# Kernel optimization log

Measured on AMD Instinct MI355X. Metric: run time of the kernel, lower is better.

## Reference

```python
import jax, jax.numpy as jnp
import numpy as np
from jax import lax

DN = ('NCHW', 'OIHW', 'NCHW')
BN_EPS = 1e-5

def conv2d(x, w, b=None, pad=0):
    y = lax.conv_general_dilated(x, w, (1, 1), [(pad, pad), (pad, pad)], dimension_numbers=DN)
    if b is not None:
        y = y + b[None, :, None, None]
    return y

def setup_inputs() -> dict:
    key = jax.random.key(0)
    ks = jax.random.split(key, 12)
    B, C, H, W = 8, 256, 64, 64
    ca = C // 4  # dim_att = 64
    s = 0.05  # weight scale to keep attention logits sane
    return {
        'x': jax.random.normal(ks[0], (B, C, H, W), jnp.float32),
        'w_dw1': jax.random.normal(ks[1], (ca // 2, ca, 7, 7), jnp.float32) * s,
        'b_dw1': jax.random.normal(ks[2], (ca // 2,), jnp.float32) * s,
        'w_dw2': jax.random.normal(ks[3], (ca // 2, ca, 11, 11), jnp.float32) * s,
        'b_dw2': jax.random.normal(ks[4], (ca // 2,), jnp.float32) * s,
        'w_k': jax.random.normal(ks[5], (ca, ca, 1, 1), jnp.float32) * s,
        'b_k': jax.random.normal(ks[6], (ca,), jnp.float32) * s,
        'w_v': jax.random.normal(ks[7], (ca, ca, 1, 1), jnp.float32) * s,
        'b_v': jax.random.normal(ks[8], (ca,), jnp.float32) * s,
        'w_c1': jax.random.normal(ks[9], (C, C, 1, 1), jnp.float32) * s,
        'bn_g': jnp.ones((C,), jnp.float32),
        'bn_b': jnp.zeros((C,), jnp.float32),
        'bn_m': jnp.zeros((C,), jnp.float32),
        'bn_var': jnp.ones((C,), jnp.float32),
        'w_c2': jax.random.normal(ks[10], (C, C, 1, 1), jnp.float32) * s,
        'b_c2': jax.random.normal(ks[11], (C,), jnp.float32) * s,
    }

def reference(x, w_dw1, b_dw1, w_dw2, b_dw2, w_k, b_k, w_v, b_v,
              w_c1, bn_g, bn_b, bn_m, bn_var, w_c2, b_c2):
    ca = w_k.shape[0]  # dim_att
    B, C, H, W = x.shape
    HW = H * W
    x1 = x[:, :ca]
    x2 = x[:, ca:]
    # Q from two multi-scale convs (7x7 and 11x11, same padding)
    q = jnp.concatenate([conv2d(x1, w_dw1, b_dw1, pad=3),
                         conv2d(x1, w_dw2, b_dw2, pad=5)], axis=1)  # [B,ca,H,W]
    q = q.reshape(B, ca, HW)                                         # [B,ca,HW]
    k = conv2d(x1, w_k, b_k).reshape(B, ca, HW)                      # [B,ca,HW]
    v = conv2d(x1, w_v, b_v).reshape(B, ca, HW)                      # [B,ca,HW]
    # att[b,n,m] = softmax_m( sum_c q[b,c,n] * k[b,c,m] )
    att = jax.nn.softmax(jnp.einsum('bcn,bcm->bnm', q, k), axis=-1)  # [B,HW,HW]
    # out1[b,c,n] = sum_m v[b,c,m] * att[b,n,m]
    out1 = jnp.einsum('bcm,bnm->bcn', v, att).reshape(B, ca, H, W)
    y = jnp.concatenate([out1, x2], axis=1)  # [B,C,H,W]
    # conv1 = YOLO Conv: 1x1 conv (no bias) + BatchNorm (eval stats) + SiLU
    y = conv2d(y, w_c1)
    inv = lax.rsqrt(bn_var + BN_EPS)
    y = (y - bn_m[None, :, None, None]) * (bn_g * inv)[None, :, None, None] + bn_b[None, :, None, None]
    y = jax.nn.silu(y)
    # conv2 = plain 1x1 conv with bias
    return conv2d(y, w_c2, b_c2)
```

## Files before the change

### kernel.cpp

```cpp
#include <hip/hip_runtime.h>

typedef __attribute__((ext_vector_type(8))) short frag8;
typedef __attribute__((ext_vector_type(4))) float f32x4;
typedef __attribute__((ext_vector_type(8))) unsigned short us8;
typedef __attribute__((ext_vector_type(4))) unsigned short us4;
typedef __attribute__((ext_vector_type(2))) unsigned int u32x2;

#define MFMA(a,b,c) __builtin_amdgcn_mfma_f32_16x16x32_bf16((a),(b),(c),0,0,0)
#define LOG2E 1.44269504f
#define EXP2(x) __builtin_amdgcn_exp2f(x)

__device__ __forceinline__ unsigned short f2bf(float f){
  unsigned int u = __builtin_bit_cast(unsigned int, f);
  u += 0x7fffu + ((u >> 16) & 1u);
  return (unsigned short)(u >> 16);
}

__device__ __forceinline__ float bf2f(unsigned short h){
  unsigned int u = ((unsigned int)h) << 16;
  return __builtin_bit_cast(float, u);
}

__device__ __forceinline__ unsigned int cvt_pk_bf16(float a, float b){
  unsigned int r;
  asm volatile("v_cvt_pk_bf16_f32 %0, %1, %2" : "=v"(r) : "v"(a), "v"(b));
  return r;
}

#define OFF_XT   ((size_t)0)
#define OFF_KT   ((size_t)16777216)
#define OFF_VCT  ((size_t)20971520)
#define OFF_QT   ((size_t)25165824)
#define OFF_O1T  ((size_t)29360128)
#define OFF_ZT   ((size_t)33554432)
#define OFF_WQ7  ((size_t)50331648)
#define OFF_WQ11 ((size_t)50532352)
#define OFF_WC1  ((size_t)51027968)
#define OFF_WC2  ((size_t)51159040)
#define OFF_BC1  ((size_t)51290112)
#define OFF_WKB  ((size_t)51291136)
#define OFF_WVB  ((size_t)51299328)
#define OFF_ML2  OFF_WQ7
#define OFF_ML4  ((size_t)51307520)
#define WS_NEED4 ((size_t)(OFF_ML4 + 1048576))

__global__ __launch_bounds__(256) void prep_weights_kernel(
    const float* __restrict__ wdw1, const float* __restrict__ wdw2,
    const float* __restrict__ wc1, const float* __restrict__ bng,
    const float* __restrict__ bnb, const float* __restrict__ bnm,
    const float* __restrict__ bnv, const float* __restrict__ wc2,
    const float* __restrict__ wk, const float* __restrict__ wv,
    unsigned short* __restrict__ wq7, unsigned short* __restrict__ wq11,
    unsigned short* __restrict__ wc1b, unsigned short* __restrict__ wc2b,
    float* __restrict__ bc1, unsigned short* __restrict__ wkb,
    unsigned short* __restrict__ wvb){
  int i = blockIdx.x*256 + threadIdx.x;
  if (i < 100352){
    int o = i >> 11, rem = i & 2047;
    int co = rem >> 6, ci = rem & 63;
    int kh = o / 7, kw = o % 7;
    wq7[i] = f2bf(wdw1[(co*64 + ci)*49 + kh*7 + kw]);
  } else if (i < 348160){
    int j = i - 100352;
    int o = j >> 11, rem = j & 2047;
    int co = rem >> 6, ci = rem & 63;
    int kh = o / 11, kw = o % 11;
    wq11[j] = f2bf(wdw2[(co*64 + ci)*121 + kh*11 + kw]);
  } else if (i < 413696){
    int j = i - 348160;
    int co = j >> 8;
    float a = bng[co] * rsqrtf(bnv[co] + 1e-5f);
    wc1b[j] = f2bf(wc1[j] * a);
    if ((j & 255) == 0) bc1[co] = bnb[co] - bnm[co]*a;
  } else if (i < 479232){
    int j = i - 413696;
    wc2b[j] = f2bf(wc2[j]);
  } else if (i < 483328){
    int j = i - 479232;
    wkb[j] = f2bf(wk[j]);
  } else if (i < 487424){
    int j = i - 483328;
    wvb[j] = f2bf(wv[j]);
  }
}

__global__ __launch_bounds__(256) void prep_x_kernel(const float* __restrict__ x,
                                                     unsigned short* __restrict__ xt){
  int g = blockIdx.x*256 + threadIdx.x;
  int b = g >> 12, n = g & 4095;
  int c0base = blockIdx.y * 64;
  const float* xp = x + (((size_t)b*256) << 12) + n;
  unsigned short* op = xt + (size_t)g*256;
  for (int c0 = c0base; c0 < c0base + 64; c0 += 8){
    us8 v;
    #pragma unroll
    for (int j = 0; j < 8; ++j) v[j] = f2bf(xp[(size_t)(c0+j) << 12]);
    *reinterpret_cast<us8*>(op + c0) = v;
  }
}

__global__ __launch_bounds__(256) void kv_kernel(const unsigned short* __restrict__ xt,
    const unsigned short* __restrict__ wkb, const unsigned short* __restrict__ wvb,
    const float* __restrict__ bk, const float* __restrict__ bv,
    unsigned short* __restrict__ kt, unsigned short* __restrict__ vct){
  int gid = blockIdx.x;
  int part = gid >> 9, t = gid & 511;
  int b = t >> 6, tile = t & 63;
  int lane = threadIdx.x & 63, wid = threadIdx.x >> 6;
  int lo = lane & 15, hi = lane >> 4;
  int n0 = tile*64 + wid*16;
  size_t bb = (size_t)b << 12;
  f32x4 acc[4];
  #pragma unroll
  for (int f = 0; f < 4; ++f) acc[f] = (f32x4){0.f,0.f,0.f,0.f};
  frag8 x0 = *reinterpret_cast<const frag8*>(xt + (bb + n0 + lo)*256 + 8*hi);
  frag8 x1 = *reinterpret_cast<const frag8*>(xt + (bb + n0 + lo)*256 + 32 + 8*hi);
  if (part == 0){
    #pragma unroll
    for (int nf = 0; nf < 4; ++nf){
      frag8 w0 = *reinterpret_cast<const frag8*>(wkb + (nf*16 + lo)*64 + 8*hi);
      frag8 w1 = *reinterpret_cast<const frag8*>(wkb + (nf*16 + lo)*64 + 32 + 8*hi);
      acc[nf] = MFMA(x0, w0, acc[nf]);
      acc[nf] = MFMA(x1, w1, acc[nf]);
    }
    #pragma unroll
    for (int nf = 0; nf < 4; ++nf){
      int co = nf*16 + lo;
      float bias = bk[co];
      #pragma unroll
      for (int r = 0; r < 4; ++r)
        kt[(bb + n0 + hi*4 + r)*64 + co] = f2bf(acc[nf][r] + bias);
    }
  } else {
    #pragma unroll
    for (int mf = 0; mf < 4; ++mf){
      frag8 w0 = *reinterpret_cast<const frag8*>(wvb + (mf*16 + lo)*64 + 8*hi);
      frag8 w1 = *reinterpret_cast<const frag8*>(wvb + (mf*16 + lo)*64 + 32 + 8*hi);
      acc[mf] = MFMA(w0, x0, acc[mf]);
      acc[mf] = MFMA(w1, x1, acc[mf]);
    }
    #pragma unroll
    for (int mf = 0; mf < 4; ++mf){
      #pragma unroll
      for (int r = 0; r < 4; ++r){
        int c = mf*16 + hi*4 + r;
        vct[(((size_t)b*64 + c) << 12) + n0 + lo] = f2bf(acc[mf][r] + bv[c]);
      }
    }
  }
}

template<int KS>
__global__ __launch_bounds__(256) void conv_q_kernel(const unsigned short* __restrict__ xt,
    const unsigned short* __restrict__ wq, const float* __restrict__ bias,
    unsigned short* __restrict__ qt){
  constexpr int P = KS/2;
  constexpr int NR = (KS+1)/2;
  __shared__ unsigned short xs[NR*64*64];
  __shared__ float outst[2][64][33];
  int h0 = blockIdx.x*2, b = blockIdx.y;
  int tid = threadIdx.x, lane = tid & 63, wid = tid >> 6;
  int lo = lane & 15, hi = lane >> 4;
  int cofrag = wid & 1, hsel = wid >> 1;
  int h = h0 + hsel;
  f32x4 acc[4];
  #pragma unroll
  for (int nf = 0; nf < 4; ++nf) acc[nf] = (f32x4){0.f,0.f,0.f,0.f};
  const size_t xbase = ((size_t)b << 12) * 256;
  #pragma unroll
  for (int pass = 0; pass < 2; ++pass){
    const int srcBase = h0 - P + pass*NR;
    if (pass) __syncthreads();
    for (int idx = tid; idx < NR*512; idx += 256){
      int rl = idx >> 9, w = (idx >> 3) & 63, ch = idx & 7;
      int sr = srcBase + rl;
      us8 v = {0,0,0,0,0,0,0,0};
      if (sr >= 0 && sr < 64)
        v = *reinterpret_cast<const us8*>(xt + xbase + (size_t)(sr*64 + w)*256 + ch*8);
      int byte = (rl*64 + w)*128 + ((ch*16) ^ ((w & 7) << 4));
      *reinterpret_cast<us8*>((char*)xs + byte) = v;
    }
    __syncthreads();
    for (int rl = 0; rl < NR; ++rl){
      int dh = srcBase + rl - h + P;
      if (dh < 0 || dh >= KS) continue;
      frag8 wf[KS][2];
      int off0 = dh*KS;
      #pragma unroll
      for (int dw = 0; dw < KS; ++dw){
        #pragma unroll
        for (int ks = 0; ks < 2; ++ks)
          wf[dw][ks] = *reinterpret_cast<const frag8*>(
              wq + (size_t)(off0+dw)*2048 + (cofrag*16 + lo)*64 + ks*32 + 8*hi);
      }
      #pragma unroll
      for (int dw = 0; dw < KS; ++dw){
        #pragma unroll
        for (int nf = 0; nf < 4; ++nf){
          int w_out = nf*16 + lo;
          int wp = w_out + dw - P;
          frag8 bx0 = {0,0,0,0,0,0,0,0}, bx1 = {0,0,0,0,0,0,0,0};
          if (wp >= 0 && wp < 64){
            int rowb = (rl*64 + wp)*128;
            int sw = (wp & 7) << 4;
            bx0 = *reinterpret_cast<const frag8*>((char*)xs + rowb + ((hi*16) ^ sw));
            bx1 = *reinterpret_cast<const frag8*>((char*)xs + rowb + ((64 + hi*16) ^ sw));
          }
          acc[nf] = MFMA(wf[dw][0], bx0, acc[nf]);
          acc[nf] = MFMA(wf[dw][1], bx1, acc[nf]);
        }
      }
    }
  }
  #pragma unroll
  for (int nf = 0; nf < 4; ++nf){
    int w = nf*16 + lo;
    #pragma unroll
    for (int r = 0; r < 4; ++r)
      outst[hsel][w][cofrag*16 + hi*4 + r] = acc[nf][r];
  }
  __syncthreads();
  {
    int hs = tid >> 7, rem = tid & 127;
    int w = rem >> 1, c16 = (rem & 1)*16;
    int cobase = (KS == 7) ? 0 : 32;
    size_t qrow = (((size_t)b << 12) + (h0 + hs)*64 + w)*64;
    #pragma unroll
    for (int g = 0; g < 2; ++g){
      int c8 = c16 + g*8;
      us8 v;
      #pragma unroll
      for (int j = 0; j < 8; ++j)
        v[j] = f2bf((outst[hs][w][c8 + j] + bias[c8 + j]) * LOG2E);
      *reinterpret_cast<us8*>(qt + qrow + cobase + c8) = v;
    }
  }
}

template<int NSPLIT>
__global__ __launch_bounds__(256, 2) void attn_kernel(const unsigned short* __restrict__ qt,
    const unsigned short* __restrict__ kt, const unsigned short* __restrict__ vct,
    unsigned short* __restrict__ opart, float* __restrict__ mlpart){
  constexpr int TILES = 64 / NSPLIT;
  __shared__ unsigned short kls[2][64*64];
  __shared__ unsigned short vls[2][64*64];
  __shared__ unsigned short pls[4][32*64];
  int b = blockIdx.y, half = blockIdx.z;
  int tid = threadIdx.x, lane = tid & 63, wid = tid >> 6;
  int lo = lane & 15, hi = lane >> 4;
  int q0 = blockIdx.x*128 + wid*32;
  const size_t bb = (size_t)b << 12;
  const int mtbase = half * TILES;
  const int sm = tid >> 3, sch = tid & 7;
  const int dstA = sm*128 + ((sch*16) ^ ((sm & 7) << 4));
  const int dstB = dstA + 32*128;
  char* pbase = (char*)pls[wid];
  frag8 aq[2][2];
  #pragma unroll
  for (int mf = 0; mf < 2; ++mf)
    #pragma unroll
    for (int ks = 0; ks < 2; ++ks)
      aq[mf][ks] = *reinterpret_cast<const frag8*>(
          qt + (bb + q0 + mf*16 + lo)*64 + ks*32 + 8*hi);
  f32x4 o[2][4];
  #pragma unroll
  for (int mf = 0; mf < 2; ++mf)
    #pragma unroll
    for (int f = 0; f < 4; ++f) o[mf][f] = (f32x4){0.f,0.f,0.f,0.f};
  float mr[2]  = {-1e30f, -1e30f};
  float lr[2]  = {0.f, 0.f};
  float mrT[2][4];
  #pragma unroll
  for (int mf = 0; mf < 2; ++mf)
    #pragma unroll
    for (int r = 0; r < 4; ++r) mrT[mf][r] = -1e30f;
  us8 kr0, kr1, vr0, vr1;
  {
    int mt = mtbase;
    kr0 = *reinterpret_cast<const us8*>(kt + (bb + mt*64 + sm)*64 + sch*8);
    kr1 = *reinterpret_cast<const us8*>(kt + (bb + mt*64 + sm + 32)*64 + sch*8);
    vr0 = *reinterpret_cast<const us8*>(vct + (((size_t)b*64 + sm) << 12) + mt*64 + sch*8);
    vr1 = *reinterpret_cast<const us8*>(vct + (((size_t)b*64 + sm + 32) << 12) + mt*64 + sch*8);
    *reinterpret_cast<us8*>((char*)kls[0] + dstA) = kr0;
    *reinterpret_cast<us8*>((char*)kls[0] + dstB) = kr1;
    *reinterpret_cast<us8*>((char*)vls[0] + dstA) = vr0;
    *reinterpret_cast<us8*>((char*)vls[0] + dstB) = vr1;
  }
  __syncthreads();
  int cur = 0;
  for (int t = 0; t < TILES; ++t){
    if (t < TILES-1){
      int mt = mtbase + t + 1;
      kr0 = *reinterpret_cast<const us8*>(kt + (bb + mt*64 + sm)*64 + sch*8);
      kr1 = *reinterpret_cast<const us8*>(kt + (bb + mt*64 + sm + 32)*64 + sch*8);
      vr0 = *reinterpret_cast<const us8*>(vct + (((size_t)b*64 + sm) << 12) + mt*64 + sch*8);
      vr1 = *reinterpret_cast<const us8*>(vct + (((size_t)b*64 + sm + 32) << 12) + mt*64 + sch*8);
    }
    f32x4 s[2][4];
    #pragma unroll
    for (int mf = 0; mf < 2; ++mf)
      #pragma unroll
      for (int f = 0; f < 4; ++f) s[mf][f] = (f32x4){0.f,0.f,0.f,0.f};
    #pragma unroll
    for (int nf = 0; nf < 4; ++nf){
      int m = nf*16 + lo;
      int sw = (m & 7) << 4;
      frag8 b0 = *reinterpret_cast<const frag8*>((char*)kls[cur] + m*128 + ((hi*16) ^ sw));
      frag8 b1 = *reinterpret_cast<const frag8*>((char*)kls[cur] + m*128 + ((64 + hi*16) ^ sw));
      s[0][nf] = MFMA(b0, aq[0][0], s[0][nf]);
      s[0][nf] = MFMA(b1, aq[0][1], s[0][nf]);
      s[1][nf] = MFMA(b0, aq[1][0], s[1][nf]);
      s[1][nf] = MFMA(b1, aq[1][1], s[1][nf]);
    }
    float pm[2];
    #pragma unroll
    for (int mf = 0; mf < 2; ++mf){
      float a0 = fmaxf(fmaxf(s[mf][0][0], s[mf][0][1]), fmaxf(s[mf][0][2], s[mf][0][3]));
      float a1 = fmaxf(fmaxf(s[mf][1][0], s[mf][1][1]), fmaxf(s[mf][1][2], s[mf][1][3]));
      float a2 = fmaxf(fmaxf(s[mf][2][0], s[mf][2][1]), fmaxf(s[mf][2][2], s[mf][2][3]));
      float a3 = fmaxf(fmaxf(s[mf][3][0], s[mf][3][1]), fmaxf(s[mf][3][2], s[mf][3][3]));
      pm[mf] = fmaxf(fmaxf(a0, a1), fmaxf(a2, a3));
    }
    float growth = fmaxf(pm[0] - mr[0], pm[1] - mr[1]);
    if (!__all(growth <= 11.5416f)){
      float rmax[2] = {pm[0], pm[1]};
      #pragma unroll
      for (int mf = 0; mf < 2; ++mf){
        rmax[mf] = fmaxf(rmax[mf], __shfl_xor(rmax[mf], 16));
        rmax[mf] = fmaxf(rmax[mf], __shfl_xor(rmax[mf], 32));
        float mn = fmaxf(mr[mf], rmax[mf]);
        lr[mf] *= EXP2(mr[mf] - mn);
        mr[mf] = mn;
      }
      #pragma unroll
      for (int mf = 0; mf < 2; ++mf)
        #pragma unroll
        for (int r = 0; r < 4; ++r){
          float mnT = __shfl(mr[mf], hi*4 + r);
          float scT = EXP2(mrT[mf][r] - mnT);
          mrT[mf][r] = mnT;
          #pragma unroll
          for (int cf = 0; cf < 4; ++cf) o[mf][cf][r] *= scT;
        }
    }
    #pragma unroll
    for (int mf = 0; mf < 2; ++mf){
      float acc = 0.f;
      #pragma unroll
      for (int nf = 0; nf < 4; ++nf){
        #pragma unroll
        for (int r = 0; r < 4; ++r){
          s[mf][nf][r] = EXP2(s[mf][nf][r] - mr[mf]);
          acc += s[mf][nf][r];
        }
        u32x2 w;
        w[0] = cvt_pk_bf16(s[mf][nf][0], s[mf][nf][1]);
        w[1] = cvt_pk_bf16(s[mf][nf][2], s[mf][nf][3]);
        *reinterpret_cast<u32x2*>(pbase + (mf*16 + lo)*128 +
            ((nf*32 + hi*8) ^ ((lo & 7) << 4))) = w;
      }
      lr[mf] += acc;
    }
    #pragma unroll
    for (int ks = 0; ks < 2; ++ks){
      frag8 ap0 = *reinterpret_cast<const frag8*>(
          pbase + lo*128 + ((ks*64 + hi*16) ^ ((lo & 7) << 4)));
      frag8 ap1 = *reinterpret_cast<const frag8*>(
          pbase + (16 + lo)*128 + ((ks*64 + hi*16) ^ ((lo & 7) << 4)));
      #pragma unroll
      for (int cf = 0; cf < 4; ++cf){
        int c = cf*16 + lo;
        frag8 bv = *reinterpret_cast<const frag8*>(
            (char*)vls[cur] + c*128 + ((ks*64 + hi*16) ^ ((c & 7) << 4)));
        o[0][cf] = MFMA(ap0, bv, o[0][cf]);
        o[1][cf] = MFMA(ap1, bv, o[1][cf]);
      }
    }
    if (t < TILES-1){
      *reinterpret_cast<us8*>((char*)kls[cur^1] + dstA) = kr0;
      *reinterpret_cast<us8*>((char*)kls[cur^1] + dstB) = kr1;
      *reinterpret_cast<us8*>((char*)vls[cur^1] + dstA) = vr0;
      *reinterpret_cast<us8*>((char*)vls[cur^1] + dstB) = vr1;
    }
    __syncthreads();
    cur ^= 1;
  }
  #pragma unroll
  for (int mf = 0; mf < 2; ++mf){
    lr[mf] += __shfl_xor(lr[mf], 16);
    lr[mf] += __shfl_xor(lr[mf], 32);
  }
  size_t pb = ((size_t)(half*8 + b) << 12);
  #pragma unroll
  for (int mf = 0; mf < 2; ++mf){
    #pragma unroll
    for (int cf = 0; cf < 4; ++cf)
      #pragma unroll
      for (int r = 0; r < 4; ++r)
        opart[(pb + q0 + mf*16 + hi*4 + r)*64 + cf*16 + lo] = f2bf(o[mf][cf][r]);
    if (hi == 0){
      size_t idx = pb + q0 + mf*16 + lo;
      mlpart[idx*2]     = mr[mf];
      mlpart[idx*2 + 1] = lr[mf];
    }
  }
}

template<int NSPLIT>
__global__ __launch_bounds__(256) void merge_kernel(const unsigned short* __restrict__ opart,
    const float* __restrict__ mlpart, unsigned short* __restrict__ o1t){
  int g = blockIdx.x*256 + threadIdx.x;
  int c4 = g & 15, q = (g >> 4) & 4095, b = g >> 16;
  size_t idx[NSPLIT];
  float m[NSPLIT], l[NSPLIT];
  float M = -1e30f;
  #pragma unroll
  for (int p = 0; p < NSPLIT; ++p){
    idx[p] = ((size_t)(p*8 + b) << 12) + q;
    m[p] = mlpart[idx[p]*2];
    l[p] = mlpart[idx[p]*2 + 1];
    M = fmaxf(M, m[p]);
  }
  float denom = 0.f, w[NSPLIT];
  #pragma unroll
  for (int p = 0; p < NSPLIT; ++p){
    w[p] = EXP2(m[p] - M);
    denom += w[p] * l[p];
  }
  float inv = 1.0f / denom;
  f32x4 acc = (f32x4){0.f,0.f,0.f,0.f};
  #pragma unroll
  for (int p = 0; p < NSPLIT; ++p){
    us4 a = *reinterpret_cast<const us4*>(opart + idx[p]*64 + c4*4);
    float wp = w[p] * inv;
    #pragma unroll
    for (int j = 0; j < 4; ++j) acc[j] += wp * bf2f(a[j]);
  }
  unsigned short outv[4];
  #pragma unroll
  for (int j = 0; j < 4; ++j) outv[j] = f2bf(acc[j]);
  *reinterpret_cast<ulonglong1*>(o1t + (((size_t)b << 12) + q)*64 + c4*4) =
      *reinterpret_cast<ulonglong1*>(outv);
}

__global__ __launch_bounds__(256) void c1_kernel(const unsigned short* __restrict__ o1t,
    const unsigned short* __restrict__ xt, const unsigned short* __restrict__ wc1b,
    const float* __restrict__ bc1, unsigned short* __restrict__ zt){
  int b = blockIdx.y;
  int q0 = blockIdx.x*64 + (threadIdx.x >> 6)*16;
  int lane = threadIdx.x & 63, lo = lane & 15, hi = lane >> 4;
  size_t bb = (size_t)b << 12;
  f32x4 acc[16];
  #pragma unroll
  for (int nf = 0; nf < 16; ++nf) acc[nf] = (f32x4){0.f,0.f,0.f,0.f};
  #pragma unroll
  for (int ks = 0; ks < 8; ++ks){
    int ci0 = ks*32 + 8*hi;
    frag8 a;
    if (ks < 2) a = *reinterpret_cast<const frag8*>(o1t + (bb + q0 + lo)*64 + ci0);
    else        a = *reinterpret_cast<const frag8*>(xt  + (bb + q0 + lo)*256 + ci0);
    #pragma unroll
    for (int nf = 0; nf < 16; ++nf){
      frag8 w = *reinterpret_cast<const frag8*>(wc1b + (nf*16 + lo)*256 + ci0);
      acc[nf] = MFMA(a, w, acc[nf]);
    }
  }
  #pragma unroll
  for (int nf = 0; nf < 16; ++nf){
    int co = nf*16 + lo;
    float bias = bc1[co];
    #pragma unroll
    for (int r = 0; r < 4; ++r){
      float y = acc[nf][r] + bias;
      y = y / (1.0f + __expf(-y));
      zt[(bb + q0 + hi*4 + r)*256 + co] = f2bf(y);
    }
  }
}

__global__ __launch_bounds__(256) void c2_kernel(const unsigned short* __restrict__ zt,
    const unsigned short* __restrict__ wc2b, const float* __restrict__ bc2,
    float* __restrict__ out){
  int b = blockIdx.y;
  int q0 = blockIdx.x*128 + (threadIdx.x >> 6)*32;
  int lane = threadIdx.x & 63, lo = lane & 15, hi = lane >> 4;
  size_t bb = (size_t)b << 12;
  f32x4 acc[16][2];
  #pragma unroll
  for (int mf = 0; mf < 16; ++mf){
    acc[mf][0] = (f32x4){0.f,0.f,0.f,0.f};
    acc[mf][1] = (f32x4){0.f,0.f,0.f,0.f};
  }
  #pragma unroll
  for (int ks = 0; ks < 8; ++ks){
    int ci0 = ks*32 + 8*hi;
    frag8 bz0 = *reinterpret_cast<const frag8*>(zt + (bb + q0 + lo)*256 + ci0);
    frag8 bz1 = *reinterpret_cast<const frag8*>(zt + (bb + q0 + 16 + lo)*256 + ci0);
    #pragma unroll
    for (int mf = 0; mf < 16; ++mf){
      frag8 aw = *reinterpret_cast<const frag8*>(wc2b + (mf*16 + lo)*256 + ci0);
      acc[mf][0] = MFMA(aw, bz0, acc[mf][0]);
      acc[mf][1] = MFMA(aw, bz1, acc[mf][1]);
    }
  }
  #pragma unroll
  for (int mf = 0; mf < 16; ++mf){
    #pragma unroll
    for (int r = 0; r < 4; ++r){
      int co = mf*16 + hi*4 + r;
      float bias = bc2[co];
      float* op = out + (((size_t)b*256 + co) << 12) + q0 + lo;
      op[0]  = acc[mf][0][r] + bias;
      op[16] = acc[mf][1][r] + bias;
    }
  }
}

extern "C" void kernel_launch(void* const* d_in, const int* in_sizes, int n_in,
                              void* d_out, int out_size, void* d_ws, size_t ws_size,
                              hipStream_t stream){
  const float* x    = (const float*)d_in[0];
  const float* wdw1 = (const float*)d_in[1];
  const float* bdw1 = (const float*)d_in[2];
  const float* wdw2 = (const float*)d_in[3];
  const float* bdw2 = (const float*)d_in[4];
  const float* wk   = (const float*)d_in[5];
  const float* bk   = (const float*)d_in[6];
  const float* wv   = (const float*)d_in[7];
  const float* bv   = (const float*)d_in[8];
  const float* wc1  = (const float*)d_in[9];
  const float* bng  = (const float*)d_in[10];
  const float* bnb  = (const float*)d_in[11];
  const float* bnm  = (const float*)d_in[12];
  const float* bnv  = (const float*)d_in[13];
  const float* wc2  = (const float*)d_in[14];
  const float* bc2  = (const float*)d_in[15];
  char* ws = (char*)d_ws;
  unsigned short* xt   = (unsigned short*)(ws + OFF_XT);
  unsigned short* ktp  = (unsigned short*)(ws + OFF_KT);
  unsigned short* vct  = (unsigned short*)(ws + OFF_VCT);
  unsigned short* qtp  = (unsigned short*)(ws + OFF_QT);
  unsigned short* o1t  = (unsigned short*)(ws + OFF_O1T);
  unsigned short* zt   = (unsigned short*)(ws + OFF_ZT);
  unsigned short* wq7  = (unsigned short*)(ws + OFF_WQ7);
  unsigned short* wq11 = (unsigned short*)(ws + OFF_WQ11);
  unsigned short* wc1b = (unsigned short*)(ws + OFF_WC1);
  unsigned short* wc2b = (unsigned short*)(ws + OFF_WC2);
  float*          bc1  = (float*)(ws + OFF_BC1);
  unsigned short* wkb  = (unsigned short*)(ws + OFF_WKB);
  unsigned short* wvb  = (unsigned short*)(ws + OFF_WVB);
  unsigned short* opart = (unsigned short*)(ws + OFF_ZT);
  const bool big = (ws_size >= WS_NEED4);
  float*          mlp   = (float*)(ws + (big ? OFF_ML4 : OFF_ML2));

  prep_weights_kernel<<<1904, 256, 0, stream>>>(wdw1, wdw2, wc1, bng, bnb, bnm, bnv,
                                                wc2, wk, wv, wq7, wq11, wc1b, wc2b,
                                                bc1, wkb, wvb);
  prep_x_kernel<<<dim3(128, 4), 256, 0, stream>>>(x, xt);
  kv_kernel<<<1024, 256, 0, stream>>>(xt, wkb, wvb, bk, bv, ktp, vct);
  conv_q_kernel<7><<<dim3(32, 8), 256, 0, stream>>>(xt, wq7, bdw1, qtp);
  conv_q_kernel<11><<<dim3(32, 8), 256, 0, stream>>>(xt, wq11, bdw2, qtp);
  if (big){
    attn_kernel<4><<<dim3(32, 8, 4), 256, 0, stream>>>(qtp, ktp, vct, opart, mlp);
    merge_kernel<4><<<2048, 256, 0, stream>>>(opart, mlp, o1t);
  } else {
    attn_kernel<2><<<dim3(32, 8, 2), 256, 0, stream>>>(qtp, ktp, vct, opart, mlp);
    merge_kernel<2><<<2048, 256, 0, stream>>>(opart, mlp, o1t);
  }
  c1_kernel<<<dim3(64, 8), 256, 0, stream>>>(o1t, xt, wc1b, bc1, zt);
  c2_kernel<<<dim3(32, 8), 256, 0, stream>>>(zt, wc2b, bc2, (float*)d_out);
}
```

Before: 230.5 us.

## Fuse split-softmax merge into c1 GEMM and merge both Q convs into one launch

The merge of the split-attention partial outputs now happens inside the c1 1x1-conv kernel, which reads the partial outputs and their max/sum stats directly when building the first two K-slices of the A operand. This removes one kernel launch and the write and re-read of the o1t buffer. The 7x7 and 11x11 Q convolutions are also combined into one launch with 64 x-blocks, which lets them run concurrently. Shared memory is now sized for the larger 11x11 case in every block. The c1 output is redirected into the K buffer region to avoid aliasing opart.

```diff
diff --git a/kernel.cpp b/kernel.cpp
--- a/kernel.cpp
+++ b/kernel.cpp
@@ -151,14 +151,12 @@
 }
 
 template<int KS>
-__global__ __launch_bounds__(256) void conv_q_kernel(const unsigned short* __restrict__ xt,
+__device__ __forceinline__ void conv_body(const unsigned short* __restrict__ xt,
     const unsigned short* __restrict__ wq, const float* __restrict__ bias,
-    unsigned short* __restrict__ qt){
+    unsigned short* __restrict__ qt, int h0, int b,
+    unsigned short* xs, float* outst ){
   constexpr int P = KS/2;
   constexpr int NR = (KS+1)/2;
-  __shared__ unsigned short xs[NR*64*64];
-  __shared__ float outst[2][64][33];
-  int h0 = blockIdx.x*2, b = blockIdx.y;
   int tid = threadIdx.x, lane = tid & 63, wid = tid >> 6;
   int lo = lane & 15, hi = lane >> 4;
   int cofrag = wid & 1, hsel = wid >> 1;
@@ -217,7 +215,7 @@
     int w = nf*16 + lo;
     #pragma unroll
     for (int r = 0; r < 4; ++r)
-      outst[hsel][w][cofrag*16 + hi*4 + r] = acc[nf][r];
+      outst[(hsel*64 + w)*33 + cofrag*16 + hi*4 + r] = acc[nf][r];
   }
   __syncthreads();
   {
@@ -231,10 +229,22 @@
       us8 v;
       #pragma unroll
       for (int j = 0; j < 8; ++j)
-        v[j] = f2bf((outst[hs][w][c8 + j] + bias[c8 + j]) * LOG2E);
+        v[j] = f2bf((outst[(hs*64 + w)*33 + c8 + j] + bias[c8 + j]) * LOG2E);
       *reinterpret_cast<us8*>(qt + qrow + cobase + c8) = v;
     }
   }
+}
+
+__global__ __launch_bounds__(256) void conv_q_both_kernel(
+    const unsigned short* __restrict__ xt,
+    const unsigned short* __restrict__ wq7, const unsigned short* __restrict__ wq11,
+    const float* __restrict__ b7, const float* __restrict__ b11,
+    unsigned short* __restrict__ qt){
+  __shared__ unsigned short xs[6*64*64];
+  __shared__ float outst[2*64*33];
+  int bx = blockIdx.x, b = blockIdx.y;
+  if (bx < 32) conv_body<7>(xt, wq7, b7, qt, bx*2, b, xs, outst);
+  else         conv_body<11>(xt, wq11, b11, qt, (bx-32)*2, b, xs, outst);
 }
 
 template<int NSPLIT>
@@ -407,49 +417,34 @@
 }
 
 template<int NSPLIT>
-__global__ __launch_bounds__(256) void merge_kernel(const unsigned short* __restrict__ opart,
-    const float* __restrict__ mlpart, unsigned short* __restrict__ o1t){
-  int g = blockIdx.x*256 + threadIdx.x;
-  int c4 = g & 15, q = (g >> 4) & 4095, b = g >> 16;
-  size_t idx[NSPLIT];
-  float m[NSPLIT], l[NSPLIT];
-  float M = -1e30f;
-  #pragma unroll
-  for (int p = 0; p < NSPLIT; ++p){
-    idx[p] = ((size_t)(p*8 + b) << 12) + q;
-    m[p] = mlpart[idx[p]*2];
-    l[p] = mlpart[idx[p]*2 + 1];
-    M = fmaxf(M, m[p]);
-  }
-  float denom = 0.f, w[NSPLIT];
-  #pragma unroll
-  for (int p = 0; p < NSPLIT; ++p){
-    w[p] = EXP2(m[p] - M);
-    denom += w[p] * l[p];
-  }
-  float inv = 1.0f / denom;
-  f32x4 acc = (f32x4){0.f,0.f,0.f,0.f};
-  #pragma unroll
-  for (int p = 0; p < NSPLIT; ++p){
-    us4 a = *reinterpret_cast<const us4*>(opart + idx[p]*64 + c4*4);
-    float wp = w[p] * inv;
-    #pragma unroll
-    for (int j = 0; j < 4; ++j) acc[j] += wp * bf2f(a[j]);
-  }
-  unsigned short outv[4];
-  #pragma unroll
-  for (int j = 0; j < 4; ++j) outv[j] = f2bf(acc[j]);
-  *reinterpret_cast<ulonglong1*>(o1t + (((size_t)b << 12) + q)*64 + c4*4) =
-      *reinterpret_cast<ulonglong1*>(outv);
-}
-
-__global__ __launch_bounds__(256) void c1_kernel(const unsigned short* __restrict__ o1t,
-    const unsigned short* __restrict__ xt, const unsigned short* __restrict__ wc1b,
-    const float* __restrict__ bc1, unsigned short* __restrict__ zt){
+__global__ __launch_bounds__(256) void c1m_kernel(const unsigned short* __restrict__ opart,
+    const float* __restrict__ mlpart, const unsigned short* __restrict__ xt,
+    const unsigned short* __restrict__ wc1b, const float* __restrict__ bc1,
+    unsigned short* __restrict__ zt){
   int b = blockIdx.y;
   int q0 = blockIdx.x*64 + (threadIdx.x >> 6)*16;
   int lane = threadIdx.x & 63, lo = lane & 15, hi = lane >> 4;
   size_t bb = (size_t)b << 12;
+  int q = q0 + lo;
+  size_t idxp[NSPLIT];
+  float m[NSPLIT], l[NSPLIT];
+  float M = -1e30f;
+  #pragma unroll
+  for (int p = 0; p < NSPLIT; ++p){
+    idxp[p] = ((size_t)(p*8 + b) << 12) + q;
+    m[p] = mlpart[idxp[p]*2];
+    l[p] = mlpart[idxp[p]*2 + 1];
+    M = fmaxf(M, m[p]);
+  }
+  float denom = 0.f, wp[NSPLIT];
+  #pragma unroll
+  for (int p = 0; p < NSPLIT; ++p){
+    wp[p] = EXP2(m[p] - M);
+    denom += wp[p] * l[p];
+  }
+  float inv = 1.0f / denom;
+  #pragma unroll
+  for (int p = 0; p < NSPLIT; ++p) wp[p] *= inv;
   f32x4 acc[16];
   #pragma unroll
   for (int nf = 0; nf < 16; ++nf) acc[nf] = (f32x4){0.f,0.f,0.f,0.f};
@@ -457,8 +452,21 @@
   for (int ks = 0; ks < 8; ++ks){
     int ci0 = ks*32 + 8*hi;
     frag8 a;
-    if (ks < 2) a = *reinterpret_cast<const frag8*>(o1t + (bb + q0 + lo)*64 + ci0);
-    else        a = *reinterpret_cast<const frag8*>(xt  + (bb + q0 + lo)*256 + ci0);
+    if (ks < 2){
+      float av[8] = {0.f,0.f,0.f,0.f,0.f,0.f,0.f,0.f};
+      #pragma unroll
+      for (int p = 0; p < NSPLIT; ++p){
+        us8 ap = *reinterpret_cast<const us8*>(opart + idxp[p]*64 + ci0);
+        #pragma unroll
+        for (int j = 0; j < 8; ++j) av[j] += wp[p] * bf2f(ap[j]);
+      }
+      union { unsigned u[4]; frag8 f; } pk;
+      #pragma unroll
+      for (int j = 0; j < 4; ++j) pk.u[j] = cvt_pk_bf16(av[2*j], av[2*j+1]);
+      a = pk.f;
+    } else {
+      a = *reinterpret_cast<const frag8*>(xt + (bb + q0 + lo)*256 + ci0);
+    }
     #pragma unroll
     for (int nf = 0; nf < 16; ++nf){
       frag8 w = *reinterpret_cast<const frag8*>(wc1b + (nf*16 + lo)*256 + ci0);
@@ -540,7 +548,6 @@
   unsigned short* ktp  = (unsigned short*)(ws + OFF_KT);
   unsigned short* vct  = (unsigned short*)(ws + OFF_VCT);
   unsigned short* qtp  = (unsigned short*)(ws + OFF_QT);
-  unsigned short* o1t  = (unsigned short*)(ws + OFF_O1T);
   unsigned short* zt   = (unsigned short*)(ws + OFF_ZT);
   unsigned short* wq7  = (unsigned short*)(ws + OFF_WQ7);
   unsigned short* wq11 = (unsigned short*)(ws + OFF_WQ11);
@@ -552,21 +559,21 @@
   unsigned short* opart = (unsigned short*)(ws + OFF_ZT);
   const bool big = (ws_size >= WS_NEED4);
   float*          mlp   = (float*)(ws + (big ? OFF_ML4 : OFF_ML2));
+  unsigned short* ztx  = (unsigned short*)(ws + OFF_KT);
 
   prep_weights_kernel<<<1904, 256, 0, stream>>>(wdw1, wdw2, wc1, bng, bnb, bnm, bnv,
                                                 wc2, wk, wv, wq7, wq11, wc1b, wc2b,
                                                 bc1, wkb, wvb);
   prep_x_kernel<<<dim3(128, 4), 256, 0, stream>>>(x, xt);
   kv_kernel<<<1024, 256, 0, stream>>>(xt, wkb, wvb, bk, bv, ktp, vct);
-  conv_q_kernel<7><<<dim3(32, 8), 256, 0, stream>>>(xt, wq7, bdw1, qtp);
-  conv_q_kernel<11><<<dim3(32, 8), 256, 0, stream>>>(xt, wq11, bdw2, qtp);
+  conv_q_both_kernel<<<dim3(64, 8), 256, 0, stream>>>(xt, wq7, wq11, bdw1, bdw2, qtp);
   if (big){
     attn_kernel<4><<<dim3(32, 8, 4), 256, 0, stream>>>(qtp, ktp, vct, opart, mlp);
-    merge_kernel<4><<<2048, 256, 0, stream>>>(opart, mlp, o1t);
+    c1m_kernel<4><<<dim3(64, 8), 256, 0, stream>>>(opart, mlp, xt, wc1b, bc1, ztx);
   } else {
     attn_kernel<2><<<dim3(32, 8, 2), 256, 0, stream>>>(qtp, ktp, vct, opart, mlp);
-    merge_kernel<2><<<2048, 256, 0, stream>>>(opart, mlp, o1t);
-  }
-  c1_kernel<<<dim3(64, 8), 256, 0, stream>>>(o1t, xt, wc1b, bc1, zt);
-  c2_kernel<<<dim3(32, 8), 256, 0, stream>>>(zt, wc2b, bc2, (float*)d_out);
-}
+    c1m_kernel<2><<<dim3(64, 8), 256, 0, stream>>>(opart, mlp, xt, wc1b, bc1, ztx);
+  }
+  c2_kernel<<<dim3(32, 8), 256, 0, stream>>>(ztx, wc2b, bc2, (float*)d_out);
+  (void)zt;
+}
```

Measured after the change: 220.1 us. 4.5% less time.
